# Optimization experiments

Measured on AMD Instinct MI355X. Metric: run time of the kernel, lower is better.

Reference implementation:

```python
import jax, jax.numpy as jnp
import numpy as np

B, C, H, W = 16, 256, 64, 64
K = 16      # dim_k
HEADS = 4   # h
U = 1       # dim_intra
V = 64      # dim_out // heads
R = 7       # local receptive field


def setup_inputs() -> dict:
    key = jax.random.key(0)
    ks = jax.random.split(key, 6)
    dim_out = HEADS * V
    std_q = (K * dim_out) ** -0.5
    std_kv = dim_out ** -0.5
    fan_in = U * R * R
    bound = 1.0 / np.sqrt(fan_in)
    return {
        "x": jax.random.normal(ks[0], (B, C, H, W), jnp.float32),
        "Wq": jax.random.normal(ks[1], (K * HEADS, C), jnp.float32) * std_q,
        "Wk": jax.random.normal(ks[2], (K * U, C), jnp.float32) * std_kv,
        "Wv": jax.random.normal(ks[3], (V * U, C), jnp.float32) * std_kv,
        "gamma_q": jnp.ones((K * HEADS,), jnp.float32),
        "beta_q": jnp.zeros((K * HEADS,), jnp.float32),
        "gamma_v": jnp.ones((V * U,), jnp.float32),
        "beta_v": jnp.zeros((V * U,), jnp.float32),
        "pos_w": jax.random.uniform(ks[4], (K, U, R, R), jnp.float32, -bound, bound),
        "pos_b": jax.random.uniform(ks[5], (K,), jnp.float32, -bound, bound),
    }


def _bn(t, gamma, beta, eps=1e-5):
    # BatchNorm2d, training-mode batch statistics (biased variance)
    mu = t.mean(axis=(0, 2, 3), keepdims=True)
    var = ((t - mu) ** 2).mean(axis=(0, 2, 3), keepdims=True)
    return (t - mu) * jax.lax.rsqrt(var + eps) * gamma[None, :, None, None] + beta[None, :, None, None]


def reference(x, Wq, Wk, Wv, gamma_q, beta_q, gamma_v, beta_v, pos_w, pos_b):
    b, c, hh, ww = x.shape
    n = hh * ww
    # 1x1 conv projections == channel matmuls
    q = _bn(jnp.einsum('oc,bchw->bohw', Wq, x), gamma_q, beta_q)
    k = jnp.einsum('oc,bchw->bohw', Wk, x)
    v = _bn(jnp.einsum('oc,bchw->bohw', Wv, x), gamma_v, beta_v)

    q = q.reshape(b, HEADS, K, n)                 # b h k n
    k = jax.nn.softmax(k.reshape(b, U, K, n), axis=-1)  # softmax over positions m
    v4 = v.reshape(b, U, V, n)                    # b u v m

    # content lambda
    lambda_c = jnp.einsum('bukm,buvm->bkv', k, v4)
    y_c = jnp.einsum('bhkn,bkv->bhvn', q, lambda_c)

    # positional lambda: Conv3d with kernel (1,R,R) == 2D conv applied per v-slice
    v5 = v4.reshape(b, U, V, hh, ww).transpose(0, 2, 1, 3, 4).reshape(b * V, U, hh, ww)
    lp = jax.lax.conv_general_dilated(
        v5, pos_w, window_strides=(1, 1), padding='SAME',
        dimension_numbers=('NCHW', 'OIHW', 'NCHW'))
    lp = lp + pos_b[None, :, None, None]
    lp = lp.reshape(b, V, K, n).transpose(0, 2, 1, 3)  # b k v n
    y_p = jnp.einsum('bhkn,bkvn->bhvn', q, lp)

    Y = y_c + y_p                                  # b h v n
    return Y.reshape(b, HEADS * V, hh, ww)
```

## Files before the change

kernel.cpp:

```cpp
#include <hip/hip_runtime.h>

#define B_ 16
#define C_ 256
#define N_ 4096
#define NT_ 65536
#define MH_ 240

typedef _Float16 f16x8 __attribute__((ext_vector_type(8)));
typedef _Float16 f16x4 __attribute__((ext_vector_type(4)));
typedef _Float16 f16x2 __attribute__((ext_vector_type(2)));
typedef float    f32x4 __attribute__((ext_vector_type(4)));

__device__ __forceinline__ float waveSum(float v){
  #pragma unroll
  for (int off = 32; off > 0; off >>= 1) v += __shfl_xor(v, off, 64);
  return v;
}

__global__ void k_pack_w(const float* __restrict__ Wq, const float* __restrict__ Wk,
                         const float* __restrict__ Wv, const float* __restrict__ pos_w,
                         _Float16* __restrict__ Wcat, float* __restrict__ wsumq){
  int idx = blockIdx.x * 256 + threadIdx.x;
  int row = idx >> 8, col = idx & 255;
  float v;
  if (row < 64)      v = Wq[row * 256 + col];
  else if (row < 80) v = Wk[(row - 64) * 256 + col];
  else               v = Wv[(row - 80) * 256 + col];
  Wcat[idx] = (_Float16)v;
  if (idx < 16){
    float s = 0.f;
    for (int t = 0; t < 49; ++t) s += pos_w[idx * 49 + t];
    wsumq[idx] = s;
  }
}

__global__ __launch_bounds__(256) void k_proj(const float* __restrict__ x,
                                              const _Float16* __restrict__ Wcat,
                                              _Float16* __restrict__ q16,
                                              _Float16* __restrict__ v16,
                                              _Float16* __restrict__ ek16,
                                              float* __restrict__ bnpart,
                                              float* __restrict__ kpart){
  __shared__ float bsumW[4][128];
  __shared__ float bssqW[4][128];
  __shared__ float ksumW[4][16];

  const int lane = threadIdx.x & 63;
  const int wid  = threadIdx.x >> 6;
  const int tile = blockIdx.x * 4 + wid;
  const int j0 = tile << 4;
  const int b  = j0 >> 12;
  const int n0 = j0 & 4095;
  const int cl = lane & 15;
  const int kg = lane >> 4;

  f32x4 acc[9];
  #pragma unroll
  for (int m = 0; m < 9; ++m){ acc[m][0]=0.f; acc[m][1]=0.f; acc[m][2]=0.f; acc[m][3]=0.f; }

  const float* xb = x + (size_t)b * C_ * N_ + n0 + cl;
  #pragma unroll
  for (int kk = 0; kk < 8; ++kk){
    const int kb = kk * 32 + kg * 8;
    f16x8 bfrag;
    #pragma unroll
    for (int jj = 0; jj < 8; ++jj) bfrag[jj] = (_Float16)xb[(size_t)(kb + jj) * N_];
    #pragma unroll
    for (int m = 0; m < 9; ++m){
      f16x8 afrag = *reinterpret_cast<const f16x8*>(Wcat + ((m * 16 + cl) << 8) + kb);
      acc[m] = __builtin_amdgcn_mfma_f32_16x16x32_f16(afrag, bfrag, acc[m], 0, 0, 0);
    }
  }

  {
    float eks[4];
    f16x4 h4;
    #pragma unroll
    for (int r = 0; r < 4; ++r){ eks[r] = __expf(acc[4][r]); h4[r] = (_Float16)eks[r]; }
    *reinterpret_cast<f16x4*>(ek16 + (((size_t)(j0 + cl)) << 4) + kg * 4) = h4;
    #pragma unroll
    for (int r = 0; r < 4; ++r){
      #pragma unroll
      for (int off = 1; off < 16; off <<= 1) eks[r] += __shfl_xor(eks[r], off, 64);
      if (cl == 0) ksumW[wid][kg * 4 + r] = eks[r];
    }
  }

  const size_t prow = ((size_t)(j0 + cl)) << 6;
  #pragma unroll
  for (int m = 0; m < 4; ++m){
    f16x4 h4;
    #pragma unroll
    for (int r = 0; r < 4; ++r) h4[r] = (_Float16)acc[m][r];
    *reinterpret_cast<f16x4*>(q16 + prow + m * 16 + kg * 4) = h4;
  }
  #pragma unroll
  for (int m = 5; m < 9; ++m){
    f16x4 h4;
    #pragma unroll
    for (int r = 0; r < 4; ++r) h4[r] = (_Float16)acc[m][r];
    *reinterpret_cast<f16x4*>(v16 + prow + (m - 5) * 16 + kg * 4) = h4;
  }

  #pragma unroll
  for (int m = 0; m < 9; ++m){
    if (m == 4) continue;
    #pragma unroll
    for (int r = 0; r < 4; ++r){
      float sv = acc[m][r];
      float sq = sv * sv;
      #pragma unroll
      for (int off = 1; off < 16; off <<= 1){
        sv += __shfl_xor(sv, off, 64);
        sq += __shfl_xor(sq, off, 64);
      }
      if (cl == 0){
        int idx = ((m < 4) ? m * 16 : (m - 5) * 16 + 64) + kg * 4 + r;
        bsumW[wid][idx] = sv;
        bssqW[wid][idx] = sq;
      }
    }
  }
  __syncthreads();
  if (threadIdx.x < 128){
    int i = threadIdx.x;
    float s  = bsumW[0][i] + bsumW[1][i] + bsumW[2][i] + bsumW[3][i];
    float sq = bssqW[0][i] + bssqW[1][i] + bssqW[2][i] + bssqW[3][i];
    bnpart[(size_t)i * 1024 + blockIdx.x]         = s;
    bnpart[(size_t)(i + 128) * 1024 + blockIdx.x] = sq;
  } else if (threadIdx.x < 144){
    int t = threadIdx.x - 128;
    float s = ksumW[0][t] + ksumW[1][t] + ksumW[2][t] + ksumW[3][t];
    kpart[(size_t)((blockIdx.x >> 6) * 16 + t) * 64 + (blockIdx.x & 63)] = s;
  }
}

__global__ void k_bn2(const float* __restrict__ bnpart, const float* __restrict__ kpart,
                      const float* __restrict__ gq, const float* __restrict__ bq,
                      const float* __restrict__ gv, const float* __restrict__ bv,
                      float* __restrict__ stats, float* __restrict__ kstat){
  if (blockIdx.x == 128){
    int t = threadIdx.x;
    float s = 0.f;
    #pragma unroll
    for (int i = 0; i < 64; ++i) s += kpart[(size_t)t * 64 + i];
    kstat[t] = 1.f / s;
    return;
  }
  const int ch = blockIdx.x;
  const int t = threadIdx.x;
  float s = 0.f, ss = 0.f;
  #pragma unroll
  for (int k = 0; k < 4; ++k){
    int bk = t + k * 256;
    s  += bnpart[(size_t)ch * 1024 + bk];
    ss += bnpart[(size_t)(ch + 128) * 1024 + bk];
  }
  __shared__ float r0[4], r1[4];
  const int lane = t & 63, wid = t >> 6;
  s = waveSum(s); ss = waveSum(ss);
  if (lane == 0){ r0[wid] = s; r1[wid] = ss; }
  __syncthreads();
  if (t == 0){
    s  = r0[0] + r0[1] + r0[2] + r0[3];
    ss = r1[0] + r1[1] + r1[2] + r1[3];
    float mean = s * (1.f / NT_);
    float var  = ss * (1.f / NT_) - mean * mean;
    float rs = rsqrtf(var + 1e-5f);
    if (ch < 64){
      float a = rs * gq[ch];
      stats[ch] = a; stats[64 + ch] = bq[ch] - mean * a;
    } else {
      int v = ch - 64;
      float a = rs * gv[v];
      stats[128 + v] = a; stats[192 + v] = bv[v] - mean * a;
    }
  }
}

__global__ __launch_bounds__(256) void k_lam1(const _Float16* __restrict__ ek16,
                          const _Float16* __restrict__ v16,
                          const float* __restrict__ kstat,
                          float* __restrict__ lc_part){
  const int blk = blockIdx.x;
  const int b = blk >> 6, sl = blk & 63;
  const int tid = threadIdx.x;
  const int kc = tid >> 4, vg = tid & 15;
  __shared__ float skb[16][65];

  const size_t base = (size_t)b * N_ + sl * 64;
  if (tid < 128){
    int px = tid >> 1, part = tid & 1;
    f16x8 e8 = *reinterpret_cast<const f16x8*>(ek16 + ((base + px) << 4) + part * 8);
    #pragma unroll
    for (int j = 0; j < 8; ++j)
      skb[part * 8 + j][px] = (float)e8[j] * kstat[b * 16 + part * 8 + j];
  }
  __syncthreads();

  float S0 = 0.f, S1 = 0.f, S2 = 0.f, S3 = 0.f;
  const _Float16* vbase = v16 + (base << 6) + vg * 4;
  #pragma unroll 8
  for (int j = 0; j < 64; ++j){
    f16x4 v4 = *reinterpret_cast<const f16x4*>(vbase + ((size_t)j << 6));
    float sk = skb[kc][j];
    S0 += sk * (float)v4[0];
    S1 += sk * (float)v4[1];
    S2 += sk * (float)v4[2];
    S3 += sk * (float)v4[3];
  }
  float4 w; w.x = S0; w.y = S1; w.z = S2; w.w = S3;
  *reinterpret_cast<float4*>(lc_part + (size_t)blk * 1024 + kc * 64 + vg * 4) = w;
}

__global__ void k_makeW(const float* __restrict__ stats, const float* __restrict__ lc_part,
                        const float* __restrict__ pos_w, const float* __restrict__ pos_b,
                        const float* __restrict__ wsumq,
                        _Float16* __restrict__ Wbig2, float* __restrict__ Bbig2){
  const int b = blockIdx.x >> 2, qr = blockIdx.x & 3;
  __shared__ float lcq[16][64];
  for (int o = threadIdx.x; o < 1024; o += 256){
    int kc = o >> 6, v = o & 63;
    float s = 0.f;
    for (int sl = 0; sl < 64; ++sl) s += lc_part[(size_t)(b * 64 + sl) * 1024 + o];
    lcq[kc][v] = stats[128 + v] * s + stats[192 + v] + pos_b[kc];
  }
  __syncthreads();

  const int idx = qr * 120 + threadIdx.x;
  if (threadIdx.x >= 120 || idx >= 480) return;
  const int half = idx / MH_, r = idx % MH_;
  const int rowg = (b * 2 + half) * MH_ + r;
  _Float16* wrow = Wbig2 + ((size_t)rowg << 5);
  float bias = 0.f;
  if (r < 100){
    const int h_ = (r < 98) ? (r / 49) : (r - 98);
    const int h = half * 2 + h_;
    if (r < 98){
      const int tap = r % 49;
      for (int c2 = 0; c2 < 32; ++c2){
        int qc = half * 32 + c2;
        wrow[c2] = (_Float16)(((c2 >> 4) == h_) ? stats[qc] * pos_w[(qc & 15) * 49 + tap] : 0.f);
      }
      for (int k = 0; k < 16; ++k) bias += stats[64 + h * 16 + k] * pos_w[k * 49 + tap];
    } else {
      for (int c2 = 0; c2 < 32; ++c2){
        int qc = half * 32 + c2;
        wrow[c2] = (_Float16)(((c2 >> 4) == h_) ? stats[qc] * wsumq[qc & 15] : 0.f);
      }
      for (int k = 0; k < 16; ++k) bias += stats[64 + h * 16 + k] * wsumq[k];
    }
  } else if (r < 112){
    for (int c2 = 0; c2 < 32; ++c2) wrow[c2] = (_Float16)0.f;
  } else {
    const int t = r - 112, h_ = t >> 6, vv = t & 63;
    const int h = half * 2 + h_;
    const int v = (((vv >> 2) & 3) << 4) | ((vv >> 4) << 2) | (vv & 3);
    for (int c2 = 0; c2 < 32; ++c2){
      int qc = half * 32 + c2;
      wrow[c2] = (_Float16)(((c2 >> 4) == h_) ? stats[qc] * lcq[qc & 15][v] : 0.f);
    }
    for (int k = 0; k < 16; ++k) bias += stats[64 + h * 16 + k] * lcq[k][v];
  }
  Bbig2[rowg] = bias;
}

__global__ __launch_bounds__(256, 2) void k_fused(
                        const _Float16* __restrict__ q16,
                        const _Float16* __restrict__ v16,
                        const float* __restrict__ stats,
                        const _Float16* __restrict__ Wbig2,
                        const float* __restrict__ Bbig2,
                        float* __restrict__ out){
  __shared__ _Float16 vn_s[220 * 64];
  __shared__ _Float16 s_s[4][16][98];

  const int zb = blockIdx.z;
  const int b = zb >> 1, ha = zb & 1;
  const int x0 = blockIdx.x * 16;
  const int y0 = blockIdx.y * 4;
  const int tid = threadIdx.x;
  const int lane = tid & 63, wid = tid >> 6;
  const int cl = lane & 15, kg = lane >> 4;
  const size_t bN = (size_t)b * N_;

  for (int idx = tid; idx < 1760; idx += 256){
    int pos = idx >> 3, c8 = (idx & 7) << 3;
    int yy = pos / 22, xx = pos - yy * 22;
    int gy = y0 + yy - 3, gx = x0 + xx - 3;
    f16x8 val;
    #pragma unroll
    for (int j = 0; j < 8; ++j) val[j] = (_Float16)0.f;
    if ((unsigned)gy < 64u && (unsigned)gx < 64u)
      val = *reinterpret_cast<const f16x8*>(v16 + ((bN + gy * 64 + gx) << 6) + c8);
    int e = (pos << 6) + c8;
    *reinterpret_cast<f16x8*>(&vn_s[e ^ ((pos & 7) << 3)]) = val;
  }

  const int pix = (y0 + wid) * 64 + x0 + cl;
  const _Float16* qp = q16 + ((bN + pix) << 6) + ha * 32;
  f16x8 bfrag = *reinterpret_cast<const f16x8*>(qp + kg * 8);
  const _Float16* Wb = Wbig2 + (((size_t)(b * 2 + ha) * MH_) << 5);
  const float* Bb = Bbig2 + (b * 2 + ha) * MH_;

  f32x4 acc[15];
  #pragma unroll
  for (int m = 0; m < 15; ++m){ acc[m][0]=0.f; acc[m][1]=0.f; acc[m][2]=0.f; acc[m][3]=0.f; }

  #pragma unroll
  for (int m = 0; m < 15; ++m){
    f16x8 a0 = *reinterpret_cast<const f16x8*>(Wb + ((m * 16 + cl) << 5) + kg * 8);
    acc[m] = __builtin_amdgcn_mfma_f32_16x16x32_f16(a0, bfrag, acc[m], 0, 0, 0);
  }

  #pragma unroll
  for (int m = 0; m < 15; ++m)
    acc[m] += *reinterpret_cast<const f32x4*>(Bb + m * 16 + kg * 4);

  const float ssum0 = __shfl(acc[6][2], cl, 64);
  const float ssum1 = __shfl(acc[6][3], cl, 64);

  #pragma unroll
  for (int m = 0; m < 7; ++m){
    #pragma unroll
    for (int r = 0; r < 4; ++r){
      const int row = m * 16 + kg * 4 + r;
      if (row < 98){
        const int pos = (row % 49) * 2 + row / 49;
        s_s[wid][cl][pos] = (_Float16)acc[m][r];
      }
    }
  }
  __syncthreads();

  f16x2 accB[2][8];
  #pragma unroll
  for (int h_ = 0; h_ < 2; ++h_)
    #pragma unroll
    for (int j = 0; j < 8; ++j){ accB[h_][j][0] = (_Float16)0.f; accB[h_][j][1] = (_Float16)0.f; }

  const _Float16* srow = &s_s[wid][cl][0];
  #pragma unroll
  for (int dy = 0; dy < 7; ++dy){
    #pragma unroll
    for (int dx = 0; dx < 7; ++dx){
      const int tap = dy * 7 + dx;
      const int pos = (wid + dy) * 22 + (cl + dx);
      f16x2 s2 = *reinterpret_cast<const f16x2*>(srow + tap * 2);
      const int esw = ((pos << 6) + (kg << 4)) ^ ((pos & 7) << 3);
      f16x8 va = *reinterpret_cast<const f16x8*>(&vn_s[esw]);
      f16x8 vb = *reinterpret_cast<const f16x8*>(&vn_s[esw ^ 8]);
      f16x2 p0 = __builtin_shufflevector(va, va, 0, 1);
      f16x2 p1 = __builtin_shufflevector(va, va, 2, 3);
      f16x2 p2 = __builtin_shufflevector(va, va, 4, 5);
      f16x2 p3 = __builtin_shufflevector(va, va, 6, 7);
      f16x2 p4 = __builtin_shufflevector(vb, vb, 0, 1);
      f16x2 p5 = __builtin_shufflevector(vb, vb, 2, 3);
      f16x2 p6 = __builtin_shufflevector(vb, vb, 4, 5);
      f16x2 p7 = __builtin_shufflevector(vb, vb, 6, 7);
      #pragma unroll
      for (int h_ = 0; h_ < 2; ++h_){
        f16x2 sh; sh[0] = s2[h_]; sh[1] = s2[h_];
        accB[h_][0] = sh * p0 + accB[h_][0];
        accB[h_][1] = sh * p1 + accB[h_][1];
        accB[h_][2] = sh * p2 + accB[h_][2];
        accB[h_][3] = sh * p3 + accB[h_][3];
        accB[h_][4] = sh * p4 + accB[h_][4];
        accB[h_][5] = sh * p5 + accB[h_][5];
        accB[h_][6] = sh * p6 + accB[h_][6];
        accB[h_][7] = sh * p7 + accB[h_][7];
      }
    }
  }

  float* ob = out + ((size_t)b * 256) * N_ + pix;
  f32x4 av[4], cv[4];
  #pragma unroll
  for (int vhi = 0; vhi < 4; ++vhi){
    av[vhi] = *reinterpret_cast<const f32x4*>(stats + 128 + kg * 16 + vhi * 4);
    cv[vhi] = *reinterpret_cast<const f32x4*>(stats + 192 + kg * 16 + vhi * 4);
  }
  #pragma unroll
  for (int h_ = 0; h_ < 2; ++h_){
    const float ss = h_ ? ssum1 : ssum0;
    #pragma unroll
    for (int vhi = 0; vhi < 4; ++vhi){
      const int m = 7 + h_ * 4 + vhi;
      #pragma unroll
      for (int r = 0; r < 4; ++r){
        const int j = vhi * 4 + r;
        const int ch = (ha * 2 + h_) * 64 + kg * 16 + j;
        const float band = (float)accB[h_][j >> 1][j & 1];
        ob[(size_t)ch * N_] = acc[m][r] + av[vhi][r] * band + cv[vhi][r] * ss;
      }
    }
  }
}

extern "C" void kernel_launch(void* const* d_in, const int* in_sizes, int n_in,
                              void* d_out, int out_size, void* d_ws, size_t ws_size,
                              hipStream_t stream){
  (void)in_sizes; (void)n_in; (void)out_size; (void)ws_size;
  const float* x  = (const float*)d_in[0];
  const float* Wq = (const float*)d_in[1];
  const float* Wk = (const float*)d_in[2];
  const float* Wv = (const float*)d_in[3];
  const float* gq = (const float*)d_in[4];
  const float* bq = (const float*)d_in[5];
  const float* gv = (const float*)d_in[6];
  const float* bv = (const float*)d_in[7];
  const float* pw = (const float*)d_in[8];
  const float* pb = (const float*)d_in[9];
  float* out = (float*)d_out;

  char* ws = (char*)d_ws;
  size_t off = 0;
  _Float16* Wcat  = (_Float16*)(ws + off);  off += 131072;
  _Float16* q16   = (_Float16*)(ws + off);  off += (size_t)NT_ * 64 * 2;
  _Float16* v16   = (_Float16*)(ws + off);  off += (size_t)NT_ * 64 * 2;
  _Float16* ek16  = (_Float16*)(ws + off);  off += (size_t)NT_ * 16 * 2;
  _Float16* Wbig2 = (_Float16*)(ws + off);  off += (size_t)B_ * 2 * MH_ * 32 * 2;
  float*    Bbig2 = (float*)(ws + off);     off += (size_t)B_ * 2 * MH_ * 4;
  float*    stats = (float*)(ws + off);     off += 1024;
  float*    kstat = (float*)(ws + off);     off += 1024;
  float*    wsumq = (float*)(ws + off);     off += 1024;
  float*    lc_part = (float*)(ws + off);   off += (size_t)1024 * 1024 * 4;
  float*    bnpart  = (float*)(ws + off);   off += (size_t)256 * 1024 * 4;
  float*    kpart   = (float*)(ws + off);   off += (size_t)256 * 64 * 4;

  k_pack_w <<<144, 256, 0, stream>>>(Wq, Wk, Wv, pw, Wcat, wsumq);
  k_proj   <<<1024, 256, 0, stream>>>(x, Wcat, q16, v16, ek16, bnpart, kpart);
  k_bn2    <<<129, 256, 0, stream>>>(bnpart, kpart, gq, bq, gv, bv, stats, kstat);
  k_lam1   <<<1024, 256, 0, stream>>>(ek16, v16, kstat, lc_part);
  k_makeW  <<<64, 256, 0, stream>>>(stats, lc_part, pw, pb, wsumq, Wbig2, Bbig2);
  dim3 g5(4, 16, 32);
  k_fused  <<<g5, 256, 0, stream>>>(q16, v16, stats, Wbig2, Bbig2, out);
}
```

Baseline: 125.7 us.

## Stage x tiles through double-buffered LDS with vectorized float4 loads in projection

```diff
diff --git a/kernel.cpp b/kernel.cpp
--- a/kernel.cpp
+++ b/kernel.cpp
@@ -41,35 +41,59 @@
                                               _Float16* __restrict__ ek16,
                                               float* __restrict__ bnpart,
                                               float* __restrict__ kpart){
+  __shared__ float xs[2][64][64];
   __shared__ float bsumW[4][128];
   __shared__ float bssqW[4][128];
   __shared__ float ksumW[4][16];
 
   const int lane = threadIdx.x & 63;
   const int wid  = threadIdx.x >> 6;
-  const int tile = blockIdx.x * 4 + wid;
-  const int j0 = tile << 4;
-  const int b  = j0 >> 12;
-  const int n0 = j0 & 4095;
+  const int b    = blockIdx.x >> 6;
+  const int n0b  = (blockIdx.x & 63) * 64;
+  const int j0   = (blockIdx.x << 6) + wid * 16;
   const int cl = lane & 15;
   const int kg = lane >> 4;
 
+  const float* xg = x + (size_t)b * C_ * N_ + n0b;
+  const int scol = cl * 4;
+
+  float4 st[4];
+  auto loadc = [&](int c){
+    #pragma unroll
+    for (int i = 0; i < 4; ++i)
+      st[i] = *reinterpret_cast<const float4*>(
+        xg + (size_t)(c * 64 + wid * 16 + i * 4 + kg) * N_ + scol);
+  };
+  auto storec = [&](int bi){
+    #pragma unroll
+    for (int i = 0; i < 4; ++i)
+      *reinterpret_cast<float4*>(&xs[bi][wid * 16 + i * 4 + kg][scol]) = st[i];
+  };
+
   f32x4 acc[9];
   #pragma unroll
   for (int m = 0; m < 9; ++m){ acc[m][0]=0.f; acc[m][1]=0.f; acc[m][2]=0.f; acc[m][3]=0.f; }
 
-  const float* xb = x + (size_t)b * C_ * N_ + n0 + cl;
-  #pragma unroll
-  for (int kk = 0; kk < 8; ++kk){
-    const int kb = kk * 32 + kg * 8;
-    f16x8 bfrag;
-    #pragma unroll
-    for (int jj = 0; jj < 8; ++jj) bfrag[jj] = (_Float16)xb[(size_t)(kb + jj) * N_];
-    #pragma unroll
-    for (int m = 0; m < 9; ++m){
-      f16x8 afrag = *reinterpret_cast<const f16x8*>(Wcat + ((m * 16 + cl) << 8) + kb);
-      acc[m] = __builtin_amdgcn_mfma_f32_16x16x32_f16(afrag, bfrag, acc[m], 0, 0, 0);
-    }
+  loadc(0); storec(0);
+  __syncthreads();
+  #pragma unroll
+  for (int c = 0; c < 4; ++c){
+    const int cur = c & 1;
+    if (c < 3) loadc(c + 1);
+    #pragma unroll
+    for (int k2 = 0; k2 < 2; ++k2){
+      f16x8 bfrag;
+      #pragma unroll
+      for (int jj = 0; jj < 8; ++jj)
+        bfrag[jj] = (_Float16)xs[cur][k2 * 32 + kg * 8 + jj][wid * 16 + cl];
+      const int kb = c * 64 + k2 * 32 + kg * 8;
+      #pragma unroll
+      for (int m = 0; m < 9; ++m){
+        f16x8 afrag = *reinterpret_cast<const f16x8*>(Wcat + ((m * 16 + cl) << 8) + kb);
+        acc[m] = __builtin_amdgcn_mfma_f32_16x16x32_f16(afrag, bfrag, acc[m], 0, 0, 0);
+      }
+    }
+    if (c < 3){ storec(cur ^ 1); __syncthreads(); }
   }
 
   {
```

Result: slower. 141.8 us (+12.8%).
